# Kernel optimization log

Measured on AMD Instinct MI355X. Metric: run time of the kernel, lower is better.

The kernel has to match this reference:

```python
import jax, jax.numpy as jnp
import numpy as np

NUM_COARSE = 1024

def sqdist(a, b):
    # a: [..., N, 3], b: [..., M, 3] -> [..., N, M] squared euclidean distances
    d = (jnp.sum(a * a, -1)[..., :, None] + jnp.sum(b * b, -1)[..., None, :]
         - 2.0 * jnp.einsum('...nd,...md->...nm', a, b))
    return jnp.maximum(d, 0.0)

def fps_idx(pts, n_samples):
    # pts: [N, 3]; farthest point sampling starting from index 0 (pn2 convention)
    d0 = jnp.sum((pts - pts[0]) ** 2, -1)  # [N]
    def step(dists, _):
        idx = jnp.argmax(dists)
        d = jnp.sum((pts - pts[idx]) ** 2, -1)
        return jnp.minimum(dists, d), idx
    _, idxs = jax.lax.scan(step, d0, None, length=n_samples - 1)
    return jnp.concatenate([jnp.zeros((1,), jnp.int32), idxs.astype(jnp.int32)])

def emd_dist(x, y, eps, iters):
    # x, y: [n, 3] equal-cardinality clouds. Approximate optimal assignment via
    # log-domain entropic OT (eps = regularization, iters = iterations), then
    # per-point squared distance to the matched point (as in the auction EMD kernel).
    n = x.shape[0]
    C = sqdist(x, y)                       # [n, n]
    Cs = jax.lax.stop_gradient(C)          # assignment is a constant wrt grads
    loga = -jnp.log(jnp.float32(n))
    def step(f, _):
        g = -eps * jax.nn.logsumexp((f[:, None] - Cs) / eps + loga, axis=0)
        f = -eps * jax.nn.logsumexp((g[None, :] - Cs) / eps + loga, axis=1)
        return f, None
    f, _ = jax.lax.scan(step, jnp.zeros((n,), Cs.dtype), None, length=iters)
    g = -eps * jax.nn.logsumexp((f[:, None] - Cs) / eps + loga, axis=0)
    assign = jnp.argmax(f[:, None] + g[None, :] - Cs, axis=1)  # [n]
    return jnp.take_along_axis(C, assign[:, None], axis=1)[:, 0]

def chamfer(a, b):
    # a: [B, N, 3], b: [B, M, 3] -> per-point min squared dists ([B,N], [B,M])
    C = sqdist(a, b)
    return jnp.min(C, axis=2), jnp.min(C, axis=1)

def setup_inputs() -> dict:
    key = jax.random.key(0)
    k1, k2, k3 = jax.random.split(key, 3)
    return {
        'output1': jax.random.uniform(k1, (4, NUM_COARSE, 3), jnp.float32),
        'output2': jax.random.uniform(k2, (4, 4096, 3), jnp.float32),
        'gt': jax.random.uniform(k3, (4, 4096, 3), jnp.float32),
        'eps': jnp.float32(0.005),
        'iters': 10,
    }

def reference(output1, output2, gt, eps, iters):
    gt = gt[:, :, :3]
    # --- EMD branch ---
    idx = jax.vmap(lambda p: fps_idx(p, NUM_COARSE))(gt)            # [B, num_coarse]
    gt_fps = jnp.take_along_axis(gt, idx[:, :, None], axis=1)       # [B, num_coarse, 3]
    d1 = jax.vmap(lambda x, y: emd_dist(x, y, eps, iters))(output1, gt_fps)
    emd1 = jnp.sqrt(d1).mean(1)
    d2 = jax.vmap(lambda x, y: emd_dist(x, y, eps, iters))(output2, gt)
    emd2 = jnp.sqrt(d2).mean(1)
    # --- Chamfer branch ---
    d11, d12 = chamfer(gt, output1)
    cd_p1 = (jnp.sqrt(d11).mean(1) + jnp.sqrt(d12).mean(1)) / 2
    cd_t1 = d11.mean(1) + d12.mean(1)
    d21, d22 = chamfer(gt, output2)
    cd_p2 = (jnp.sqrt(d21).mean(1) + jnp.sqrt(d22).mean(1)) / 2
    cd_t2 = d21.mean(1) + d22.mean(1)
    return (output1, output2, emd1, emd2, cd_p1, cd_p2, cd_t1, cd_t2)
```

## Files before the change

kernel.cpp:

```cpp
#include <hip/hip_runtime.h>
#include <math.h>


#define LOG2E 1.4426950408889634f
#define LN2   0.6931471805599453f
#define NEGBIG -3.0e38f

#define SY2(b) ((b) * 512)
#define SYF(b) (2048 + (b) * 16)

#if __has_builtin(__builtin_amdgcn_exp2f)
__device__ __forceinline__ float fexp2(float x) { return __builtin_amdgcn_exp2f(x); }
#else
__device__ __forceinline__ float fexp2(float x) { return exp2f(x); }
#endif

__device__ __forceinline__ float dist_rn(float x, float y, float z,
                                         float qx, float qy, float qz) {
  float dx = __fsub_rn(x, qx), dy = __fsub_rn(y, qy), dz = __fsub_rn(z, qz);
  return __fadd_rn(__fadd_rn(__fmul_rn(dx, dx), __fmul_rn(dy, dy)),
                   __fmul_rn(dz, dz));
}

struct FpsS {
  float4 sq[4096];
  unsigned long long xch[4][2];
  float4 sOut[64];
};
struct WorkS {
  float4 ldsRow[256];
  float4 ldsC[1024];
  float ldsG2[1024];
  float red[8];
};
struct Emd1S {
  float4 rowsO[1024];
  float4 rowsG[1024];
  float2 part[16][64];
  float g2[1024];
  float red[8];
};
union SmemAll {
  FpsS f;
  WorkS w;
  Emd1S e;
  float pad_force_one_block_per_cu[21504];
};

struct UniArgs {
  const float* gt;
  const float* epsP;
  const float4 *o1P4, *o2P4, *gtP4;
  float4* gfP4;
  float2 *gpart2, *fpart2, *apart2;
  unsigned long long* vecT;
  unsigned* sync;
  float* out;
  int NC2, BPB;
};

__device__ __forceinline__ void bar_signal(unsigned* slot, unsigned val) {
  __syncthreads();
  if (threadIdx.x == 0)
    __hip_atomic_store(slot, val, __ATOMIC_RELEASE, __HIP_MEMORY_SCOPE_AGENT);
}
template <int SLP>
__device__ __forceinline__ void bar_waitall(const unsigned* base, int n,
                                            unsigned target) {
  if (threadIdx.x < 64) {
    int l = threadIdx.x;
    for (;;) {
      unsigned v = (l < n)
                       ? __hip_atomic_load(base + l * 16, __ATOMIC_RELAXED,
                                           __HIP_MEMORY_SCOPE_AGENT)
                       : target;
      if (__all((int)(v >= target))) break;
      __builtin_amdgcn_s_sleep(SLP);
    }
    if (l == 0)
      (void)__hip_atomic_load(base, __ATOMIC_ACQUIRE, __HIP_MEMORY_SCOPE_AGENT);
  }
  __syncthreads();
}

__device__ __forceinline__ float blockRedSum(float v, float* red4) {
#pragma unroll
  for (int m = 32; m; m >>= 1) v += __shfl_xor(v, m, 64);
  int lane = threadIdx.x & 63, wid = threadIdx.x >> 6;
  __syncthreads();
  if (lane == 0) red4[wid] = v;
  __syncthreads();
  float s = 0.0f;
  if (threadIdx.x == 0) {
#pragma unroll
    for (int w = 0; w < 4; ++w) s += red4[w];
  }
  return s;
}

__global__ __launch_bounds__(256) void prep_kernel(
    const float* __restrict__ o1, const float* __restrict__ o2,
    const float* __restrict__ gt, const float* __restrict__ epsP,
    float4* __restrict__ o1P4, float4* __restrict__ o2P4,
    float4* __restrict__ gtP4) {
  int id = blockIdx.x * 256 + threadIdx.x;
  float eps = *epsP;
  float se = (1.0f / eps) * LOG2E;
  float kxy = sqrtf(se + se);
  const float* src;
  float4* dst;
  if (id < 4096) { src = o1 + 3 * id; dst = o1P4 + id; }
  else if (id < 20480) { int p = id - 4096; src = o2 + 3 * p; dst = o2P4 + p; }
  else { int p = id - 20480; src = gt + 3 * p; dst = gtP4 + p; }
  float x = src[0], y = src[1], z = src[2];
  float xx = x * x + y * y + z * z;
  *dst = make_float4(kxy * x, kxy * y, kxy * z, xx * se);
}

template <int NC>
__device__ __forceinline__ float finalize_w(const float2* __restrict__ part,
                                            int gi, int stride, float nloga2) {
  float2 pp[NC];
#pragma unroll
  for (int c = 0; c < NC; ++c) pp[c] = part[c * stride + gi];
  float m = pp[0].x;
#pragma unroll
  for (int c = 1; c < NC; ++c) m = fmaxf(m, pp[c].x);
  float s = 0.0f;
#pragma unroll
  for (int c = 0; c < NC; ++c) s += pp[c].y * fexp2(pp[c].x - m);
  return nloga2 - (m + __log2f(s));
}

template <int NC>
__device__ void pass2_job(int b, int cb, int ch, const float4* __restrict__ rowP,
                          const float4* __restrict__ colP,
                          const float2* __restrict__ vpart,
                          float2* __restrict__ dst, float4* ldsRow) {
  const int CH = 4096 / NC;
  int tid = threadIdx.x;
  int gj = b * 4096 + cb * 2048 + tid;
  float cx[8], cy[8], cz[8];
#pragma unroll
  for (int c = 0; c < 8; ++c) {
    float4 cp = colP[gj + (c << 8)];
    cx[c] = cp.x; cy[c] = cp.y; cz[c] = cp.z;
  }
  float M[8], S[8];
#pragma unroll
  for (int c = 0; c < 8; ++c) { M[c] = NEGBIG; S[c] = 0.0f; }
  int r0 = ch * CH;
  for (int t0 = 0; t0 < CH; t0 += 256) {
    __syncthreads();
    {
      int gi = b * 4096 + r0 + t0 + tid;
      float4 rp = rowP[gi];
      float w = vpart ? finalize_w<NC>(vpart, gi, 16384, 12.0f) : -rp.w;
      ldsRow[tid] = make_float4(rp.x, rp.y, rp.z, w);
    }
    __syncthreads();
#pragma unroll 1
    for (int r = 0; r < 256; r += 8) {
      float4 q[8];
#pragma unroll
      for (int u = 0; u < 8; ++u) q[u] = ldsRow[r + u];
#pragma unroll
      for (int c = 0; c < 8; ++c) {
        float t[8];
#pragma unroll
        for (int u = 0; u < 8; ++u)
          t[u] = fmaf(cx[c], q[u].x, fmaf(cy[c], q[u].y, fmaf(cz[c], q[u].z, q[u].w)));
        float cm = fmaxf(fmaxf(fmaxf(t[0], t[1]), fmaxf(t[2], t[3])),
                         fmaxf(fmaxf(t[4], t[5]), fmaxf(t[6], t[7])));
        float nM = fmaxf(M[c], cm);
        float s8 = ((fexp2(t[0] - nM) + fexp2(t[1] - nM)) +
                    (fexp2(t[2] - nM) + fexp2(t[3] - nM))) +
                   ((fexp2(t[4] - nM) + fexp2(t[5] - nM)) +
                    (fexp2(t[6] - nM) + fexp2(t[7] - nM)));
        S[c] = fmaf(S[c], fexp2(M[c] - nM), s8);
        M[c] = nM;
      }
    }
  }
#pragma unroll
  for (int c = 0; c < 8; ++c)
    dst[ch * 16384 + gj + (c << 8)] = make_float2(M[c], S[c]);
}

__device__ void cham_job(const float4* __restrict__ aP, const float4* __restrict__ bP,
                         int Na, int Nb, float* outP, float* outT,
                         float scaleP, float scaleT, int b, int rb,
                         WorkS& w, const float* epsP) {
  int tid = threadIdx.x;
  int i0 = rb * 512 + tid, i1 = i0 + 256;
  float4 a0 = aP[b * Na + i0], a1 = aP[b * Na + i1];
  float m0 = 3.0e38f, m1 = 3.0e38f;
  for (int t0 = 0; t0 < Nb; t0 += 1024) {
    __syncthreads();
    for (int t = tid; t < 1024; t += 256) w.ldsC[t] = bP[b * Nb + t0 + t];
    __syncthreads();
#pragma unroll 4
    for (int t = 0; t < 1024; ++t) {
      float4 q = w.ldsC[t];
      float c0 = fmaf(-a0.z, q.z, fmaf(-a0.y, q.y, fmaf(-a0.x, q.x, q.w + a0.w)));
      float c1 = fmaf(-a1.z, q.z, fmaf(-a1.y, q.y, fmaf(-a1.x, q.x, q.w + a1.w)));
      m0 = fminf(m0, c0);
      m1 = fminf(m1, c1);
    }
  }
  float eps = *epsP;
  float inv_se = eps * LN2;
  float d0 = fmaxf(0.0f, m0 * inv_se), d1 = fmaxf(0.0f, m1 * inv_se);
  float s1 = blockRedSum(sqrtf(d0) + sqrtf(d1), w.red);
  float s2 = blockRedSum(d0 + d1, w.red);
  if (tid == 0) {
    atomicAdd(outP, s1 * scaleP);
    atomicAdd(outT, s2 * scaleT);
  }
}

__device__ void chamfer_worker(int g, const UniArgs& A, WorkS& w) {
  for (int cj = g; cj < 104; cj += 88) {
    if (cj < 32) {
      cham_job(A.gtP4, A.o2P4, 4096, 4096, A.out + 61452 + (cj >> 3),
               A.out + 61460 + (cj >> 3), 1.0f / 8192.0f, 1.0f / 4096.0f,
               cj >> 3, cj & 7, w, A.epsP);
    } else if (cj < 64) {
      int j = cj - 32;
      cham_job(A.o2P4, A.gtP4, 4096, 4096, A.out + 61452 + (j >> 3),
               A.out + 61460 + (j >> 3), 1.0f / 8192.0f, 1.0f / 4096.0f,
               j >> 3, j & 7, w, A.epsP);
    } else if (cj < 96) {
      int j = cj - 64;
      cham_job(A.gtP4, A.o1P4, 4096, 1024, A.out + 61448 + (j >> 3),
               A.out + 61456 + (j >> 3), 1.0f / 8192.0f, 1.0f / 4096.0f,
               j >> 3, j & 7, w, A.epsP);
    } else {
      int j = cj - 96;
      cham_job(A.o1P4, A.gtP4, 1024, 4096, A.out + 61448 + (j >> 1),
               A.out + 61456 + (j >> 1), 1.0f / 2048.0f, 1.0f / 1024.0f,
               j >> 1, j & 1, w, A.epsP);
    }
  }
}

template <int NC>
__device__ void assign2_job(int b, int cc, int rb, const UniArgs& A, WorkS& w) {
  int tid = threadIdx.x;
  __syncthreads();
  for (int t = tid; t < 1024; t += 256) {
    int gjc = b * 4096 + cc * 1024 + t;
    float wv = finalize_w<NC>(A.gpart2, gjc, 16384, 12.0f);
    float4 qp = A.gtP4[gjc];
    w.ldsC[t] = make_float4(qp.x, qp.y, qp.z, wv);
    w.ldsG2[t] = wv + qp.w;
  }
  __syncthreads();
#pragma unroll
  for (int rr = 0; rr < 2; ++rr) {
    int gi = b * 4096 + rb * 512 + (rr << 8) + tid;
    float4 rp = A.o2P4[gi];
    float rx = rp.x, ry = rp.y, rz = rp.z, xw = rp.w;
    float bW = NEGBIG;
    int bj = 0;
    for (int t = 0; t < 1024; ++t) {
      float4 q = w.ldsC[t];
      float W = fmaf(rz, q.z, fmaf(ry, q.y, fmaf(rx, q.x, q.w - xw)));
      W = fminf(W, w.ldsG2[t]);
      if (W > bW) { bW = W; bj = cc * 1024 + t; }
    }
    A.apart2[cc * 16384 + gi] = make_float2(bW, __int_as_float(bj));
  }
}

__device__ void combine2_job(int b, int rb, const UniArgs& A, WorkS& w) {
  int tid = threadIdx.x;
  int gi = b * 4096 + (rb << 8) + tid;
  float bW = NEGBIG;
  int bj = 0;
#pragma unroll
  for (int c = 0; c < 4; ++c) {
    float2 p = A.apart2[c * 16384 + gi];
    if (p.x > bW) { bW = p.x; bj = __float_as_int(p.y); }
  }
  float eps = *A.epsP;
  float inv_se = eps * LN2;
  float4 rp = A.o2P4[gi];
  float4 qp = A.gtP4[b * 4096 + bj];
  float dotp = rp.x * qp.x + rp.y * qp.y + rp.z * qp.z;
  float d = fmaxf(0.0f, (rp.w + qp.w - dotp) * inv_se);
  float s = blockRedSum(sqrtf(d), w.red);
  if (tid == 0) atomicAdd(A.out + 61444 + b, s * (1.0f / 4096.0f));
}

__device__ void fps_role(const UniArgs& A, int b, FpsS& f) {
  int tid = threadIdx.x;
  const float* base = A.gt + b * 12288;
  for (int t = tid; t < 4096; t += 256) {
    float x = base[3 * t], y = base[3 * t + 1], z = base[3 * t + 2];
    f.sq[t] = make_float4(x, y, z, x * x + y * y + z * z);
  }
  if (tid < 8) ((unsigned long long*)f.xch)[tid] = 0ull;
  __syncthreads();
  float eps = *A.epsP;
  float se = (1.0f / eps) * LOG2E;
  float kxy = sqrtf(se + se);
  float4 p0 = f.sq[0];
  float px[16], py[16], pz[16], d[16];
#pragma unroll
  for (int k = 0; k < 16; ++k) {
    float4 p = f.sq[tid + (k << 8)];
    px[k] = p.x; py[k] = p.y; pz[k] = p.z;
    d[k] = dist_rn(p.x, p.y, p.z, p0.x, p0.y, p0.z);
  }
  if (tid == 0)
    f.sOut[0] = make_float4(kxy * p0.x, kxy * p0.y, kxy * p0.z, p0.w * se);
  int lane = tid & 63, w = tid >> 6;
  float qx = p0.x, qy = p0.y, qz = p0.z;
  unsigned long long* xmine = &f.xch[w][0];

#define DPPSTEP(C)                                                             \
  {                                                                            \
    unsigned ov = (unsigned)__builtin_amdgcn_update_dpp(0, (int)bvu, C, 0xf,  \
                                                        0xf, true);           \
    int oi = __builtin_amdgcn_update_dpp(0, bi, C, 0xf, 0xf, true);           \
    bool t = (ov > bvu) || ((ov == bvu) && ((unsigned)oi < (unsigned)bi));    \
    bvu = t ? ov : bvu;                                                        \
    bi = t ? oi : bi;                                                          \
  }
#define SCOMB(VV, II)                                                          \
  {                                                                            \
    unsigned _v = (unsigned)(VV);                                              \
    int _i = (II);                                                             \
    if (_v > wv || (_v == wv && _i < wi)) { wv = _v; wi = _i; }                \
  }
#define XCOMB(G)                                                               \
  {                                                                            \
    unsigned _v = (unsigned)((G) >> 32);                                       \
    int _i = (int)((unsigned)(G) & 0xFFFu);                                    \
    if (_v > bv2 || (_v == bv2 && _i < bi2)) { bv2 = _v; bi2 = _i; }          \
  }

#pragma unroll 1
  for (int s = 1; s < 1024; ++s) {
    if ((s & 63) == 0 && tid < 64)
      A.gfP4[(b << 10) + (s - 64) + tid] = f.sOut[tid];
    float tv[8]; int ti[8];
#pragma unroll
    for (int i = 0; i < 8; ++i) {
      int k0 = 2 * i, k1 = 2 * i + 1;
      float n0 = fminf(d[k0], dist_rn(px[k0], py[k0], pz[k0], qx, qy, qz));
      float n1 = fminf(d[k1], dist_rn(px[k1], py[k1], pz[k1], qx, qy, qz));
      d[k0] = n0; d[k1] = n1;
      bool t = n1 > n0;
      tv[i] = t ? n1 : n0;
      ti[i] = tid + ((t ? k1 : k0) << 8);
    }
    float uv[4]; int ui[4];
#pragma unroll
    for (int i = 0; i < 4; ++i) {
      bool t = tv[2 * i + 1] > tv[2 * i];
      uv[i] = t ? tv[2 * i + 1] : tv[2 * i];
      ui[i] = t ? ti[2 * i + 1] : ti[2 * i];
    }
    bool tA = uv[1] > uv[0];
    float vA = tA ? uv[1] : uv[0]; int iA = tA ? ui[1] : ui[0];
    bool tB = uv[3] > uv[2];
    float vB = tB ? uv[3] : uv[2]; int iB = tB ? ui[3] : ui[2];
    bool tC = vB > vA;
    float bv = tC ? vB : vA; int bi = tC ? iB : iA;
    unsigned bvu = __float_as_uint(bv);
    DPPSTEP(0xB1)
    DPPSTEP(0x4E)
    DPPSTEP(0x141)
    DPPSTEP(0x140)
    unsigned wv = (unsigned)__builtin_amdgcn_readlane((int)bvu, 0);
    int wi = __builtin_amdgcn_readlane(bi, 0);
    SCOMB(__builtin_amdgcn_readlane((int)bvu, 16), __builtin_amdgcn_readlane(bi, 16))
    SCOMB(__builtin_amdgcn_readlane((int)bvu, 32), __builtin_amdgcn_readlane(bi, 32))
    SCOMB(__builtin_amdgcn_readlane((int)bvu, 48), __builtin_amdgcn_readlane(bi, 48))
    int par = s & 1;
    unsigned tagw = (unsigned)(s & 1023);
    unsigned long long mine = ((unsigned long long)wv << 32) |
                              ((unsigned long long)tagw << 16) |
                              (unsigned long long)(unsigned)wi;
    if (lane == 0)
      __hip_atomic_store(xmine + par, mine, __ATOMIC_RELAXED,
                         __HIP_MEMORY_SCOPE_WORKGROUP);
    unsigned long long g1, g2, g3;
    for (;;) {
      g1 = __hip_atomic_load(&f.xch[(w + 1) & 3][par], __ATOMIC_RELAXED,
                             __HIP_MEMORY_SCOPE_WORKGROUP);
      g2 = __hip_atomic_load(&f.xch[(w + 2) & 3][par], __ATOMIC_RELAXED,
                             __HIP_MEMORY_SCOPE_WORKGROUP);
      g3 = __hip_atomic_load(&f.xch[(w + 3) & 3][par], __ATOMIC_RELAXED,
                             __HIP_MEMORY_SCOPE_WORKGROUP);
      if ((((unsigned)(g1 >> 16) & 1023u) == tagw) &
          (((unsigned)(g2 >> 16) & 1023u) == tagw) &
          (((unsigned)(g3 >> 16) & 1023u) == tagw))
        break;
    }
    unsigned bv2 = wv; int bi2 = wi;
    XCOMB(g1) XCOMB(g2) XCOMB(g3)
    float4 q = f.sq[bi2];
    qx = q.x; qy = q.y; qz = q.z;
    if (tid == 0)
      f.sOut[s & 63] = make_float4(kxy * qx, kxy * qy, kxy * qz, q.w * se);
  }
#undef DPPSTEP
#undef SCOMB
#undef XCOMB
  if (tid < 64) A.gfP4[(b << 10) + 960 + tid] = f.sOut[tid];
  bar_signal(A.sync + SYF(b), 1u);
}

__device__ void emd1_role(int eb, int chunk, const UniArgs& A, Emd1S& m) {
  int tid = threadIdx.x;
  bar_waitall<16>(A.sync + SYF(eb), 1, 1u);
  for (int t = tid; t < 1024; t += 256) {
    float4 p = A.o1P4[eb * 1024 + t];
    m.rowsO[t] = make_float4(p.x, p.y, p.z, -p.w);
    m.rowsG[t] = A.gfP4[eb * 1024 + t];
  }
  int lane = tid & 63, rl = tid >> 6;
  int col = chunk * 64 + lane;
  float4 cG = A.gfP4[eb * 1024 + col];
  float4 cO = A.o1P4[eb * 1024 + col];
  unsigned long long* gv = A.vecT + (eb << 10);
  unsigned long long* fv = A.vecT + 4096 + (eb << 10);

  for (int s = 1; s <= 21; ++s) {
    int odd = s & 1;
    if (s >= 2) {
      const unsigned long long* v = odd ? fv : gv;
      float4* rows = odd ? m.rowsO : m.rowsG;
      unsigned want = (unsigned)(s - 1);
      unsigned long long pv0, pv1, pv2, pv3;
      unsigned rdy = 0;
      for (;;) {
        if (!(rdy & 1u)) {
          pv0 = __hip_atomic_load(v + tid, __ATOMIC_RELAXED,
                                  __HIP_MEMORY_SCOPE_AGENT);
          if ((unsigned)(pv0 >> 32) >= want) rdy |= 1u;
        }
        if (!(rdy & 2u)) {
          pv1 = __hip_atomic_load(v + tid + 256, __ATOMIC_RELAXED,
                                  __HIP_MEMORY_SCOPE_AGENT);
          if ((unsigned)(pv1 >> 32) >= want) rdy |= 2u;
        }
        if (!(rdy & 4u)) {
          pv2 = __hip_atomic_load(v + tid + 512, __ATOMIC_RELAXED,
                                  __HIP_MEMORY_SCOPE_AGENT);
          if ((unsigned)(pv2 >> 32) >= want) rdy |= 4u;
        }
        if (!(rdy & 8u)) {
          pv3 = __hip_atomic_load(v + tid + 768, __ATOMIC_RELAXED,
                                  __HIP_MEMORY_SCOPE_AGENT);
          if ((unsigned)(pv3 >> 32) >= want) rdy |= 8u;
        }
        if (rdy == 15u) break;
        __builtin_amdgcn_s_sleep(1);
      }
      rows[tid].w = __uint_as_float((unsigned)pv0);
      rows[tid + 256].w = __uint_as_float((unsigned)pv1);
      rows[tid + 512].w = __uint_as_float((unsigned)pv2);
      rows[tid + 768].w = __uint_as_float((unsigned)pv3);
    }
    __syncthreads();
    const float4* rows = odd ? m.rowsO : m.rowsG;
    float cx = odd ? cG.x : cO.x;
    float cy = odd ? cG.y : cO.y;
    float cz = odd ? cG.z : cO.z;
#pragma unroll 1
    for (int k = 0; k < 4; ++k) {
      int ch = rl * 4 + k;
      float M = NEGBIG, S = 0.0f;
      int r0 = ch * 64;
#pragma unroll 1
      for (int r = 0; r < 64; r += 8) {
        float4 q[8];
#pragma unroll
        for (int u = 0; u < 8; ++u) q[u] = rows[r0 + r + u];
        float t8[8];
#pragma unroll
        for (int u = 0; u < 8; ++u)
          t8[u] = fmaf(cx, q[u].x, fmaf(cy, q[u].y, fmaf(cz, q[u].z, q[u].w)));
        float cm = fmaxf(fmaxf(fmaxf(t8[0], t8[1]), fmaxf(t8[2], t8[3])),
                         fmaxf(fmaxf(t8[4], t8[5]), fmaxf(t8[6], t8[7])));
        float nM = fmaxf(M, cm);
        float s8 = ((fexp2(t8[0] - nM) + fexp2(t8[1] - nM)) +
                    (fexp2(t8[2] - nM) + fexp2(t8[3] - nM))) +
                   ((fexp2(t8[4] - nM) + fexp2(t8[5] - nM)) +
                    (fexp2(t8[6] - nM) + fexp2(t8[7] - nM)));
        S = fmaf(S, fexp2(M - nM), s8);
        M = nM;
      }
      m.part[ch][lane] = make_float2(M, S);
    }
    __syncthreads();
    if (tid < 64) {
      float2 pp[16];
#pragma unroll
      for (int c = 0; c < 16; ++c) pp[c] = m.part[c][tid];
      float mm = pp[0].x;
#pragma unroll
      for (int c = 1; c < 16; ++c) mm = fmaxf(mm, pp[c].x);
      float ss = 0.0f;
#pragma unroll
      for (int c = 0; c < 16; ++c) ss += pp[c].y * fexp2(pp[c].x - mm);
      float w = 10.0f - (mm + __log2f(ss));
      unsigned long long pk = ((unsigned long long)(unsigned)s << 32) |
                              (unsigned long long)__float_as_uint(w);
      __hip_atomic_store((odd ? gv : fv) + col, pk, __ATOMIC_RELAXED,
                         __HIP_MEMORY_SCOPE_AGENT);
    }
  }
  __syncthreads();
  if (chunk != 0) return;

  for (int t = tid; t < 1024; t += 256) {
    unsigned long long pv;
    for (;;) {
      pv = __hip_atomic_load(gv + t, __ATOMIC_RELAXED,
                             __HIP_MEMORY_SCOPE_AGENT);
      if ((unsigned)(pv >> 32) >= 21u) break;
      __builtin_amdgcn_s_sleep(1);
    }
    float wv = __uint_as_float((unsigned)pv);
    float4 qp = A.gfP4[eb * 1024 + t];
    m.rowsG[t] = make_float4(qp.x, qp.y, qp.z, wv);
    m.g2[t] = wv + qp.w;
  }
  __syncthreads();
  float eps = *A.epsP;
  float inv_se = eps * LN2;
  float vsum = 0.0f;
#pragma unroll
  for (int rr = 0; rr < 4; ++rr) {
    int gi = eb * 1024 + (rr << 8) + tid;
    float4 rp = A.o1P4[gi];
    float rx = rp.x, ry = rp.y, rz = rp.z, xw = rp.w;
    float bW = NEGBIG;
    int bj = 0;
    for (int t = 0; t < 1024; ++t) {
      float4 q = m.rowsG[t];
      float W = fmaf(rz, q.z, fmaf(ry, q.y, fmaf(rx, q.x, q.w - xw)));
      W = fminf(W, m.g2[t]);
      if (W > bW) { bW = W; bj = t; }
    }
    float4 qp = A.gfP4[eb * 1024 + bj];
    float dotp = rp.x * qp.x + rp.y * qp.y + rp.z * qp.z;
    float d = fmaxf(0.0f, (rp.w + qp.w - dotp) * inv_se);
    vsum += sqrtf(d);
  }
  float s = blockRedSum(vsum, m.red);
  if (tid == 0) atomicAdd(A.out + 61440 + eb, s * (1.0f / 1024.0f));
}

__global__ __launch_bounds__(256, 1) void uni_kernel(UniArgs A) {
  __shared__ SmemAll sm;
  int bid = blockIdx.x;
  if (bid < 4) {
    fps_role(A, bid, sm.f);
    return;
  }
  int e = bid - 4;
  int W = 4 * A.BPB;
  if (e < W) {
    int b = e / A.BPB, rest = e % A.BPB;
    int cb = rest / A.NC2, ch = rest % A.NC2;
    unsigned* slots = A.sync + SY2(b);
    for (int s = 1; s <= 21; ++s) {
      const float4 *rowP, *colP;
      const float2* vp;
      float2* dst;
      if (s & 1) { rowP = A.o2P4; colP = A.gtP4; vp = (s == 1) ? nullptr : A.fpart2; dst = A.gpart2; }
      else       { rowP = A.gtP4; colP = A.o2P4; vp = A.gpart2; dst = A.fpart2; }
      if (A.NC2 == 16) pass2_job<16>(b, cb, ch, rowP, colP, vp, dst, sm.w.ldsRow);
      else             pass2_job<8>(b, cb, ch, rowP, colP, vp, dst, sm.w.ldsRow);
      bar_signal(slots + rest * 16, (unsigned)s);
      bar_waitall<16>(slots, A.BPB, (unsigned)s);
    }
    for (int j = rest; j < 32; j += A.BPB) {
      int cc = j >> 3, rb = j & 7;
      if (A.NC2 == 16) assign2_job<16>(b, cc, rb, A, sm.w);
      else             assign2_job<8>(b, cc, rb, A, sm.w);
    }
    bar_signal(slots + rest * 16, 22u);
    bar_waitall<4>(slots, A.BPB, 22u);
    if (rest < 16) combine2_job(b, rest, A, sm.w);
    return;
  }
  int g = e - W;
  chamfer_worker(g, A, sm.w);
  if (g < 64) emd1_role(g >> 4, g & 15, A, sm.e);
}

extern "C" void kernel_launch(void* const* d_in, const int* in_sizes, int n_in,
                              void* d_out, int out_size, void* d_ws, size_t ws_size,
                              hipStream_t stream) {
  (void)in_sizes; (void)n_in; (void)out_size;
  const float* o1 = (const float*)d_in[0];
  const float* o2 = (const float*)d_in[1];
  const float* gt = (const float*)d_in[2];
  const float* epsP = (const float*)d_in[3];
  float* out = (float*)d_out;
  float* ws = (float*)d_ws;

  int NC2 = 16;
  {
    size_t need16 = (size_t)(4096 + 16384 + 16384 + 65536 + 65536 + 16384 +
                             2 * (16 * 32768)) * 4;
    if (ws_size < need16) NC2 = 8;
  }
  size_t off = 0;
  unsigned* syncp = (unsigned*)(ws + off); off += 4096;
  unsigned long long* vecT = (unsigned long long*)(ws + off); off += 16384;
  float4* o1P4 = (float4*)(ws + off); off += 16384;
  float4* o2P4 = (float4*)(ws + off); off += 65536;
  float4* gtP4 = (float4*)(ws + off); off += 65536;
  float4* gfP4 = (float4*)(ws + off); off += 16384;
  float2* gpart2 = (float2*)(ws + off); off += (size_t)NC2 * 32768;
  float2* fpart2 = (float2*)(ws + off); off += (size_t)NC2 * 32768;
  float2* apart2 = fpart2;

  (void)hipMemcpyAsync(out, o1, 12288 * sizeof(float), hipMemcpyDeviceToDevice, stream);
  (void)hipMemcpyAsync(out + 12288, o2, 49152 * sizeof(float), hipMemcpyDeviceToDevice, stream);
  (void)hipMemsetAsync(out + 61440, 0, 24 * sizeof(float), stream);
  (void)hipMemsetAsync(syncp, 0, (4096 + 16384) * sizeof(float), stream);

  prep_kernel<<<144, 256, 0, stream>>>(o1, o2, gt, epsP, o1P4, o2P4, gtP4);

  UniArgs A;
  A.gt = gt; A.epsP = epsP;
  A.o1P4 = o1P4; A.o2P4 = o2P4; A.gtP4 = gtP4; A.gfP4 = gfP4;
  A.gpart2 = gpart2; A.fpart2 = fpart2; A.apart2 = apart2;
  A.vecT = vecT;
  A.sync = syncp; A.out = out;
  A.NC2 = NC2; A.BPB = 2 * NC2;
  int grid = 4 + 4 * A.BPB + 88;
  uni_kernel<<<grid, 256, 0, stream>>>(A);
}
```

Before: 1.288 ms.

## Split EMD1 final assignment across all chunk blocks and add clock-warming spin

Before, only the chunk-0 block ran the final argmax assignment, looping over all 1024 rows. Now all 16 chunk blocks each take 64 rows, split the 1024 columns across 4 waves and merge the partial argmax results through shared memory, which removes a serial tail. The polling loop is simplified into a helper that reloads all four values each spin. Blocks that finish early now busy-spin on FMAs until every EMD1 batch signals done, apparently to keep GPU clocks up. This spinning may cost power, and it could deadlock if the SYD sync slots are not zeroed before launch.

After: 1.163 ms. 9.7% less time.

```diff
diff --git a/kernel.cpp b/kernel.cpp
--- a/kernel.cpp
+++ b/kernel.cpp
@@ -8,6 +8,7 @@
 
 #define SY2(b) ((b) * 512)
 #define SYF(b) (2048 + (b) * 16)
+#define SYD(b) (2112 + (b) * 16)
 
 #if __has_builtin(__builtin_amdgcn_exp2f)
 __device__ __forceinline__ float fexp2(float x) { return __builtin_amdgcn_exp2f(x); }
@@ -96,6 +97,47 @@
     for (int w = 0; w < 4; ++w) s += red4[w];
   }
   return s;
+}
+
+__device__ __forceinline__ void poll4(const unsigned long long* v, int tid,
+                                      unsigned want, float* w0, float* w1,
+                                      float* w2, float* w3) {
+  unsigned long long p0, p1, p2, p3;
+  for (;;) {
+    p0 = __hip_atomic_load(v + tid, __ATOMIC_RELAXED, __HIP_MEMORY_SCOPE_AGENT);
+    p1 = __hip_atomic_load(v + tid + 256, __ATOMIC_RELAXED, __HIP_MEMORY_SCOPE_AGENT);
+    p2 = __hip_atomic_load(v + tid + 512, __ATOMIC_RELAXED, __HIP_MEMORY_SCOPE_AGENT);
+    p3 = __hip_atomic_load(v + tid + 768, __ATOMIC_RELAXED, __HIP_MEMORY_SCOPE_AGENT);
+    if ((unsigned)(p0 >> 32) >= want && (unsigned)(p1 >> 32) >= want &&
+        (unsigned)(p2 >> 32) >= want && (unsigned)(p3 >> 32) >= want)
+      break;
+    __builtin_amdgcn_s_sleep(1);
+  }
+  *w0 = __uint_as_float((unsigned)p0);
+  *w1 = __uint_as_float((unsigned)p1);
+  *w2 = __uint_as_float((unsigned)p2);
+  *w3 = __uint_as_float((unsigned)p3);
+}
+
+__device__ void warm_spin(const UniArgs& A) {
+  float a0 = (float)(threadIdx.x + 1), a1 = a0 + 0.5f, a2 = a0 + 1.5f,
+        a3 = a0 + 2.5f;
+  const unsigned* sy = A.sync;
+  for (;;) {
+    unsigned d0 = __hip_atomic_load(sy + SYD(0), __ATOMIC_RELAXED, __HIP_MEMORY_SCOPE_AGENT);
+    unsigned d1 = __hip_atomic_load(sy + SYD(1), __ATOMIC_RELAXED, __HIP_MEMORY_SCOPE_AGENT);
+    unsigned d2 = __hip_atomic_load(sy + SYD(2), __ATOMIC_RELAXED, __HIP_MEMORY_SCOPE_AGENT);
+    unsigned d3 = __hip_atomic_load(sy + SYD(3), __ATOMIC_RELAXED, __HIP_MEMORY_SCOPE_AGENT);
+    if ((d0 & d1 & d2 & d3) != 0u) break;
+#pragma unroll
+    for (int i = 0; i < 64; ++i) {
+      a0 = fmaf(a0, 1.0000001f, 1.0e-6f);
+      a1 = fmaf(a1, 1.0000001f, 1.0e-6f);
+      a2 = fmaf(a2, 1.0000001f, 1.0e-6f);
+      a3 = fmaf(a3, 1.0000001f, 1.0e-6f);
+    }
+  }
+  asm volatile("" ::"v"(a0), "v"(a1), "v"(a2), "v"(a3));
 }
 
 __global__ __launch_bounds__(256) void prep_kernel(
@@ -434,37 +476,12 @@
     if (s >= 2) {
       const unsigned long long* v = odd ? fv : gv;
       float4* rows = odd ? m.rowsO : m.rowsG;
-      unsigned want = (unsigned)(s - 1);
-      unsigned long long pv0, pv1, pv2, pv3;
-      unsigned rdy = 0;
-      for (;;) {
-        if (!(rdy & 1u)) {
-          pv0 = __hip_atomic_load(v + tid, __ATOMIC_RELAXED,
-                                  __HIP_MEMORY_SCOPE_AGENT);
-          if ((unsigned)(pv0 >> 32) >= want) rdy |= 1u;
-        }
-        if (!(rdy & 2u)) {
-          pv1 = __hip_atomic_load(v + tid + 256, __ATOMIC_RELAXED,
-                                  __HIP_MEMORY_SCOPE_AGENT);
-          if ((unsigned)(pv1 >> 32) >= want) rdy |= 2u;
-        }
-        if (!(rdy & 4u)) {
-          pv2 = __hip_atomic_load(v + tid + 512, __ATOMIC_RELAXED,
-                                  __HIP_MEMORY_SCOPE_AGENT);
-          if ((unsigned)(pv2 >> 32) >= want) rdy |= 4u;
-        }
-        if (!(rdy & 8u)) {
-          pv3 = __hip_atomic_load(v + tid + 768, __ATOMIC_RELAXED,
-                                  __HIP_MEMORY_SCOPE_AGENT);
-          if ((unsigned)(pv3 >> 32) >= want) rdy |= 8u;
-        }
-        if (rdy == 15u) break;
-        __builtin_amdgcn_s_sleep(1);
-      }
-      rows[tid].w = __uint_as_float((unsigned)pv0);
-      rows[tid + 256].w = __uint_as_float((unsigned)pv1);
-      rows[tid + 512].w = __uint_as_float((unsigned)pv2);
-      rows[tid + 768].w = __uint_as_float((unsigned)pv3);
+      float w0, w1, w2, w3;
+      poll4(v, tid, (unsigned)(s - 1), &w0, &w1, &w2, &w3);
+      rows[tid].w = w0;
+      rows[tid + 256].w = w1;
+      rows[tid + 512].w = w2;
+      rows[tid + 768].w = w3;
     }
     __syncthreads();
     const float4* rows = odd ? m.rowsO : m.rowsG;
@@ -516,45 +533,59 @@
     }
   }
   __syncthreads();
-  if (chunk != 0) return;
-
-  for (int t = tid; t < 1024; t += 256) {
-    unsigned long long pv;
-    for (;;) {
-      pv = __hip_atomic_load(gv + t, __ATOMIC_RELAXED,
-                             __HIP_MEMORY_SCOPE_AGENT);
-      if ((unsigned)(pv >> 32) >= 21u) break;
-      __builtin_amdgcn_s_sleep(1);
-    }
-    float wv = __uint_as_float((unsigned)pv);
-    float4 qp = A.gfP4[eb * 1024 + t];
-    m.rowsG[t] = make_float4(qp.x, qp.y, qp.z, wv);
-    m.g2[t] = wv + qp.w;
+
+  {
+    float w0, w1, w2, w3;
+    poll4(gv, tid, 21u, &w0, &w1, &w2, &w3);
+    float4 qp0 = A.gfP4[eb * 1024 + tid];
+    float4 qp1 = A.gfP4[eb * 1024 + tid + 256];
+    float4 qp2 = A.gfP4[eb * 1024 + tid + 512];
+    float4 qp3 = A.gfP4[eb * 1024 + tid + 768];
+    m.rowsG[tid] = make_float4(qp0.x, qp0.y, qp0.z, w0);
+    m.g2[tid] = w0 + qp0.w;
+    m.rowsG[tid + 256] = make_float4(qp1.x, qp1.y, qp1.z, w1);
+    m.g2[tid + 256] = w1 + qp1.w;
+    m.rowsG[tid + 512] = make_float4(qp2.x, qp2.y, qp2.z, w2);
+    m.g2[tid + 512] = w2 + qp2.w;
+    m.rowsG[tid + 768] = make_float4(qp3.x, qp3.y, qp3.z, w3);
+    m.g2[tid + 768] = w3 + qp3.w;
   }
   __syncthreads();
   float eps = *A.epsP;
   float inv_se = eps * LN2;
-  float vsum = 0.0f;
-#pragma unroll
-  for (int rr = 0; rr < 4; ++rr) {
-    int gi = eb * 1024 + (rr << 8) + tid;
-    float4 rp = A.o1P4[gi];
-    float rx = rp.x, ry = rp.y, rz = rp.z, xw = rp.w;
-    float bW = NEGBIG;
-    int bj = 0;
-    for (int t = 0; t < 1024; ++t) {
-      float4 q = m.rowsG[t];
-      float W = fmaf(rz, q.z, fmaf(ry, q.y, fmaf(rx, q.x, q.w - xw)));
-      W = fminf(W, m.g2[t]);
-      if (W > bW) { bW = W; bj = t; }
-    }
-    float4 qp = A.gfP4[eb * 1024 + bj];
+  int rw = tid & 63, qc = tid >> 6;
+  int gi = eb * 1024 + chunk * 64 + rw;
+  float4 rp = A.o1P4[gi];
+  float rx = rp.x, ry = rp.y, rz = rp.z, xw = rp.w;
+  float bW = NEGBIG;
+  int bj = 0;
+  int t0 = qc * 256;
+  for (int t = t0; t < t0 + 256; ++t) {
+    float4 q = m.rowsG[t];
+    float W = fmaf(rz, q.z, fmaf(ry, q.y, fmaf(rx, q.x, q.w - xw)));
+    W = fminf(W, m.g2[t]);
+    if (W > bW) { bW = W; bj = t; }
+  }
+  m.part[qc][rw] = make_float2(bW, __int_as_float(bj));
+  __syncthreads();
+  if (tid < 64) {
+    float2 p0 = m.part[0][tid];
+    float vb = p0.x;
+    int vj = __float_as_int(p0.y);
+#pragma unroll
+    for (int c = 1; c < 4; ++c) {
+      float2 p = m.part[c][tid];
+      if (p.x > vb) { vb = p.x; vj = __float_as_int(p.y); }
+    }
+    float4 qp = A.gfP4[eb * 1024 + vj];
     float dotp = rp.x * qp.x + rp.y * qp.y + rp.z * qp.z;
-    float d = fmaxf(0.0f, (rp.w + qp.w - dotp) * inv_se);
-    vsum += sqrtf(d);
-  }
-  float s = blockRedSum(vsum, m.red);
-  if (tid == 0) atomicAdd(A.out + 61440 + eb, s * (1.0f / 1024.0f));
+    float dd = fmaxf(0.0f, (rp.w + qp.w - dotp) * inv_se);
+    float v = sqrtf(dd);
+#pragma unroll
+    for (int mk = 32; mk; mk >>= 1) v += __shfl_xor(v, mk, 64);
+    if (tid == 0) atomicAdd(A.out + 61440 + eb, v * (1.0f / 1024.0f));
+  }
+  if (chunk == 0) bar_signal(A.sync + SYD(eb), 1u);
 }
 
 __global__ __launch_bounds__(256, 1) void uni_kernel(UniArgs A) {
@@ -589,11 +620,16 @@
     bar_signal(slots + rest * 16, 22u);
     bar_waitall<4>(slots, A.BPB, 22u);
     if (rest < 16) combine2_job(b, rest, A, sm.w);
+    warm_spin(A);
     return;
   }
   int g = e - W;
   chamfer_worker(g, A, sm.w);
-  if (g < 64) emd1_role(g >> 4, g & 15, A, sm.e);
+  if (g < 64) {
+    emd1_role(g >> 4, g & 15, A, sm.e);
+  } else {
+    warm_spin(A);
+  }
 }
 
 extern "C" void kernel_launch(void* const* d_in, const int* in_sizes, int n_in,
```
